# Optimization experiments

Hardware: AMD Instinct MI355X
Metric: run time of the kernel (lower is better)

## Reference

```python
import jax, jax.numpy as jnp
import numpy as np

N, C, H, W = 4, 128, 128, 128
G, K, PAD, DIL = 4, 3, 1, 1
P = K * K
HID = 4 * C
EPS = 1e-6


def ln(x, w, b):
    m = jnp.mean(x, -1, keepdims=True)
    v = jnp.mean((x - m) ** 2, -1, keepdims=True)
    return (x - m) * jax.lax.rsqrt(v + EPS) * w + b


def linear(x, w, b):
    return x @ w.T + b


def grid_sample_zeros(img, grid):
    # img: (B,Hi,Wi,Cc); grid: (B,L,P,2) xy in [-1,1]; bilinear, zeros padding, align_corners=False
    B, Hi, Wi, Cc = img.shape
    gx = (grid[..., 0] + 1.0) * (Wi * 0.5) - 0.5
    gy = (grid[..., 1] + 1.0) * (Hi * 0.5) - 0.5
    x0 = jnp.floor(gx)
    y0 = jnp.floor(gy)
    wx1 = gx - x0
    wy1 = gy - y0
    flat = img.reshape(B, Hi * Wi, Cc)
    Bq, L, Pq = gx.shape

    def tap(yy, xx, wgt):
        valid = (xx >= 0) & (xx <= Wi - 1) & (yy >= 0) & (yy <= Hi - 1)
        idx = (jnp.clip(yy, 0, Hi - 1) * Wi + jnp.clip(xx, 0, Wi - 1)).astype(jnp.int32)
        v = jnp.take_along_axis(flat, idx.reshape(B, L * Pq)[..., None], axis=1)
        return v.reshape(B, L, Pq, Cc) * (wgt * valid)[..., None]

    return (tap(y0, x0, (1 - wx1) * (1 - wy1))
            + tap(y0, x0 + 1, wx1 * (1 - wy1))
            + tap(y0 + 1, x0, (1 - wx1) * wy1)
            + tap(y0 + 1, x0 + 1, wx1 * wy1))


def dcn_core(x, offset, mask):
    # faithful port of dcnv3_core_pytorch (stride=1, offset_scale=1.0)
    n, h, w, c = x.shape
    gc = c // G
    xp = jnp.pad(x, ((0, 0), (PAD, PAD), (PAD, PAD), (0, 0)))
    hi, wi = h + 2 * PAD, w + 2 * PAD
    base = (DIL * (K - 1)) // 2 + 0.5
    ref_y = (base + jnp.arange(h, dtype=jnp.float32)) / hi
    ref_x = (base + jnp.arange(w, dtype=jnp.float32)) / wi
    ref = jnp.stack([jnp.broadcast_to(ref_x[None, :], (h, w)),
                     jnp.broadcast_to(ref_y[:, None], (h, w))], -1)  # (h,w,2) xy
    ks = jnp.arange(K, dtype=jnp.float32) * DIL - (DIL * (K - 1)) // 2
    gxk, gyk = jnp.meshgrid(ks, ks, indexing='ij')  # x slow, y fast (torch meshgrid order)
    grid = jnp.tile(jnp.stack([gxk / wi, gyk / hi], -1).reshape(P, 2), (G, 1))  # (G*P,2)
    sn = jnp.array([wi, hi], jnp.float32)
    loc = ref[None, :, :, None, :] + grid[None, None, None] + offset.reshape(n, h, w, G * P, 2) / sn
    sg = (2.0 * loc - 1.0).reshape(n, h * w, G, P, 2).transpose(0, 2, 1, 3, 4).reshape(n * G, h * w, P, 2)
    img = xp.reshape(n, hi, wi, G, gc).transpose(0, 3, 1, 2, 4).reshape(n * G, hi, wi, gc)
    samp = grid_sample_zeros(img, sg)  # (n*G, h*w, P, gc)
    m = mask.reshape(n, h * w, G, P).transpose(0, 2, 1, 3).reshape(n * G, h * w, P)
    out = jnp.einsum('blpc,blp->blc', samp, m)
    return out.reshape(n, G, h * w, gc).transpose(0, 2, 1, 3).reshape(n, h, w, c)


def dcn_forward(xcl, dw_w, dw_b, dwln_w, dwln_b, off_w, off_b, mask_w, mask_b, outproj_w, outproj_b):
    n, h, w, c = xcl.shape
    y = jax.lax.conv_general_dilated(xcl.transpose(0, 3, 1, 2), dw_w, (1, 1),
                                     ((PAD, PAD), (PAD, PAD)),
                                     dimension_numbers=('NCHW', 'OIHW', 'NCHW'),
                                     feature_group_count=C)
    y = y + dw_b[None, :, None, None]
    x1 = jax.nn.gelu(ln(y.transpose(0, 2, 3, 1), dwln_w, dwln_b), approximate=False)
    offset = linear(x1, off_w, off_b)
    m = jax.nn.softmax(linear(x1, mask_w, mask_b).reshape(n, h, w, G, P), -1).reshape(n, h, w, G * P)
    out = dcn_core(x1, offset, m)
    return linear(out, outproj_w, outproj_b)


def setup_inputs():
    key = jax.random.key(0)
    ks = jax.random.split(key, 8)
    s = 0.02
    return {
        "x": jax.random.normal(ks[0], (N, C, H, W), jnp.float32),
        "norm1_w": jnp.ones((C,), jnp.float32), "norm1_b": jnp.zeros((C,), jnp.float32),
        "dw_w": jax.random.normal(ks[1], (C, 1, K, K), jnp.float32) * 0.1,
        "dw_b": jnp.zeros((C,), jnp.float32),
        "dwln_w": jnp.ones((C,), jnp.float32), "dwln_b": jnp.zeros((C,), jnp.float32),
        "off_w": jax.random.normal(ks[2], (G * P * 2, C), jnp.float32) * 0.05,
        "off_b": jax.random.normal(ks[3], (G * P * 2,), jnp.float32) * 0.5,
        "mask_w": jax.random.normal(ks[4], (G * P, C), jnp.float32) * 0.05,
        "mask_b": jnp.zeros((G * P,), jnp.float32),
        "outproj_w": jax.random.normal(ks[5], (C, C), jnp.float32) * s,
        "outproj_b": jnp.zeros((C,), jnp.float32),
        "norm2_w": jnp.ones((C,), jnp.float32), "norm2_b": jnp.zeros((C,), jnp.float32),
        "fc1_w": jax.random.normal(ks[6], (HID, C), jnp.float32) * s,
        "fc1_b": jnp.zeros((HID,), jnp.float32),
        "fc2_w": jax.random.normal(ks[7], (C, HID), jnp.float32) * s,
        "fc2_b": jnp.zeros((C,), jnp.float32),
    }


def reference(x, norm1_w, norm1_b, dw_w, dw_b, dwln_w, dwln_b, off_w, off_b,
              mask_w, mask_b, outproj_w, outproj_b, norm2_w, norm2_b,
              fc1_w, fc1_b, fc2_w, fc2_b):
    # pre-norm branch (layer_scale=None, post_norm=False, res_post_norm=False, drop_path=Identity)
    xcl = ln(x.transpose(0, 2, 3, 1), norm1_w, norm1_b)  # channels_first -> channels_last LN
    d = dcn_forward(xcl, dw_w, dw_b, dwln_w, dwln_b, off_w, off_b, mask_w, mask_b, outproj_w, outproj_b)
    x = x + d.transpose(0, 3, 1, 2)
    y = ln(x.transpose(0, 2, 3, 1), norm2_w, norm2_b)
    y = linear(jax.nn.gelu(linear(y, fc1_w, fc1_b), approximate=False), fc2_w, fc2_b)
    return x + y.transpose(0, 3, 1, 2)
```

## Files before the change

### kernel.cpp

```cpp
#include <hip/hip_runtime.h>

typedef unsigned short ushort_t;
typedef short short8 __attribute__((ext_vector_type(8)));
typedef float f32x4 __attribute__((ext_vector_type(4)));
typedef ushort_t ushort8v __attribute__((ext_vector_type(8)));
typedef ushort_t ushort4v __attribute__((ext_vector_type(4)));

#define HWsz 16384
#define NHWsz 65536
#define YS 136

__device__ __forceinline__ float b2f(ushort_t u){ return __uint_as_float(((unsigned)u)<<16); }
__device__ __forceinline__ ushort_t f2b(float f){
  unsigned x = __float_as_uint(f);
  x += 0x7fffu + ((x>>16)&1u);
  return (ushort_t)(x>>16);
}
__device__ __forceinline__ float gelu_fast(float x){
  float t = x*x;
  float e = __expf(x*(1.5957691216f + 0.0713548163f*t));
  return x - x*__builtin_amdgcn_rcpf(1.0f + e);
}

#define H16(p, b) ((p)*512 + ((b) ^ (((p)&7)<<4)))
#define XSW(p, b) ((p)*256 + ((b) ^ (((p)&7)<<4)))

__global__ __launch_bounds__(256) void kW_cvt(const float* __restrict__ w1, const float* __restrict__ w2,
    const float* __restrict__ offw, const float* __restrict__ maskw, const float* __restrict__ dww,
    const float* __restrict__ pw, const float* __restrict__ offb, const float* __restrict__ mb,
    ushort_t* __restrict__ w1b, ushort_t* __restrict__ w2b, ushort_t* __restrict__ owmb,
    float* __restrict__ dwwT, ushort_t* __restrict__ pwh, ushort_t* __restrict__ pwl,
    float* __restrict__ obm){
  int i = blockIdx.x*256 + threadIdx.x;
  w1b[i] = f2b(w1[i]);
  w2b[i] = f2b(w2[i]);
  if (i < 16384){
    int row = i >> 7, k = i & 127;
    float v = 0.f;
    if (row < 72) v = offw[row*128 + k];
    else if (row < 108) v = maskw[(row-72)*128 + k];
    owmb[i] = f2b(v);
    float pv = pw[i];
    ushort_t hi = f2b(pv);
    pwh[i] = hi;
    pwl[i] = f2b(pv - b2f(hi));
  }
  if (i < 1152){
    int k = i >> 7, c = i & 127;
    dwwT[i] = dww[c*9 + k];
  }
  if (i < 128){
    obm[i] = (i < 72) ? offb[i] : ((i < 108) ? mb[i-72] : 0.f);
  }
}

__global__ __launch_bounds__(256) void kA_ln1(const float* __restrict__ x,
    const float* __restrict__ w, const float* __restrict__ b,
    ushort_t* __restrict__ xcl){
  __shared__ float tile[128*66];
  __shared__ float psum[256], psq[256];
  __shared__ float ms[64], rs[64];
  int t = threadIdx.x;
  int pos0 = blockIdx.x * 64;
  int n = pos0 >> 14, hw0 = pos0 & 16383;
  const float* xb = x + (size_t)n*128*HWsz + hw0;
  for (int i=0;i<32;i++){
    int e = i*256+t;
    int c = e>>6, p = e&63;
    tile[c*66+p] = xb[(size_t)c*HWsz + p];
  }
  __syncthreads();
  {
    int part = t>>6, p = t&63;
    float s=0.f, q=0.f;
    for (int c=part*32; c<part*32+32; c++){ float v = tile[c*66+p]; s+=v; q+=v*v; }
    psum[part*64+p]=s; psq[part*64+p]=q;
  }
  __syncthreads();
  if (t<64){
    float s=psum[t]+psum[64+t]+psum[128+t]+psum[192+t];
    float q=psq[t]+psq[64+t]+psq[128+t]+psq[192+t];
    float m = s*(1.0f/128.0f);
    float v = q*(1.0f/128.0f)-m*m;
    ms[t]=m; rs[t]=rsqrtf(v+1e-6f);
  }
  __syncthreads();
  for (int i=0;i<32;i++){
    int e = i*256+t;
    int p = e>>7, c = e&127;
    float v = (tile[c*66+p]-ms[p])*rs[p]*w[c]+b[c];
    xcl[(size_t)(pos0+p)*128 + c] = f2b(v);
  }
}

__global__ __launch_bounds__(256) void kB_dw(const ushort_t* __restrict__ xcl,
    const float* __restrict__ dwwT, const float* __restrict__ dwb,
    const float* __restrict__ lnw, const float* __restrict__ lnb,
    ushort_t* __restrict__ x1){
  __shared__ float partS[16*17], partQ[16*17];
  __shared__ float ms[16], rs[16];
  int t = threadIdx.x;
  int pos0 = blockIdx.x*16;
  int n = pos0>>14, hw0 = pos0&16383, h = hw0>>7, w0 = hw0&127;
  int pp = t>>4, l = t&15, ch0 = l*8;
  int w = w0 + pp;
  float acc[8];
  {
    float4 b0 = *(const float4*)(dwb + ch0);
    float4 b1 = *(const float4*)(dwb + ch0 + 4);
    acc[0]=b0.x; acc[1]=b0.y; acc[2]=b0.z; acc[3]=b0.w;
    acc[4]=b1.x; acc[5]=b1.y; acc[6]=b1.z; acc[7]=b1.w;
  }
  #pragma unroll
  for (int kh=0; kh<3; kh++){
    int hy = h + kh - 1;
    if ((unsigned)hy < 128u){
      #pragma unroll
      for (int kw=0; kw<3; kw++){
        int wx = w + kw - 1;
        if ((unsigned)wx < 128u){
          ushort8v xv = *(const ushort8v*)(xcl + ((size_t)(n*16384 + hy*128 + wx))*128 + ch0);
          const float* wr = dwwT + (kh*3+kw)*128 + ch0;
          float4 w0v = *(const float4*)(wr);
          float4 w1v = *(const float4*)(wr+4);
          acc[0] += b2f(xv[0])*w0v.x; acc[1] += b2f(xv[1])*w0v.y;
          acc[2] += b2f(xv[2])*w0v.z; acc[3] += b2f(xv[3])*w0v.w;
          acc[4] += b2f(xv[4])*w1v.x; acc[5] += b2f(xv[5])*w1v.y;
          acc[6] += b2f(xv[6])*w1v.z; acc[7] += b2f(xv[7])*w1v.w;
        }
      }
    }
  }
  {
    float s=0.f, q=0.f;
    #pragma unroll
    for (int j=0;j<8;j++){ s+=acc[j]; q+=acc[j]*acc[j]; }
    partS[pp*17+l]=s; partQ[pp*17+l]=q;
  }
  __syncthreads();
  {
    int p = t>>4, j = t&15;
    float s = partS[p*17+j];
    float q = partQ[p*17+j];
    s += __shfl_xor(s, 1);  q += __shfl_xor(q, 1);
    s += __shfl_xor(s, 2);  q += __shfl_xor(q, 2);
    s += __shfl_xor(s, 4);  q += __shfl_xor(q, 4);
    s += __shfl_xor(s, 8);  q += __shfl_xor(q, 8);
    if (j == 0){
      float m = s*(1.0f/128.0f);
      float var = q*(1.0f/128.0f) - m*m;
      ms[p]=m; rs[p]=rsqrtf(var+1e-6f);
    }
  }
  __syncthreads();
  {
    float m = ms[pp], r = rs[pp];
    float4 lw0 = *(const float4*)(lnw + ch0);
    float4 lw1 = *(const float4*)(lnw + ch0 + 4);
    float4 lb0 = *(const float4*)(lnb + ch0);
    float4 lb1 = *(const float4*)(lnb + ch0 + 4);
    float lw[8] = {lw0.x,lw0.y,lw0.z,lw0.w,lw1.x,lw1.y,lw1.z,lw1.w};
    float lb[8] = {lb0.x,lb0.y,lb0.z,lb0.w,lb1.x,lb1.y,lb1.z,lb1.w};
    ushort8v o;
    #pragma unroll
    for (int j=0;j<8;j++){
      float v = (acc[j]-m)*r*lw[j]+lb[j];
      o[j] = f2b(gelu_fast(v));
    }
    *(ushort8v*)(x1 + (size_t)(pos0+pp)*128 + ch0) = o;
  }
}

#define RS 120
__global__ __launch_bounds__(256) void kCD_dcn(const ushort_t* __restrict__ x1,
    const ushort_t* __restrict__ owmb, const float* __restrict__ obm,
    ushort_t* __restrict__ dcnout){
  __shared__ __align__(16) ushort_t xLb[16*YS];
  __shared__ float raw[16*RS];
  __shared__ __align__(16) float descW[576*4];
  __shared__ __align__(16) int   descO[576*4];
  int t = threadIdx.x;
  int pos0 = blockIdx.x*16;
  int n = pos0>>14, hw0 = pos0&16383, h = hw0>>7, w0 = hw0&127;
  const size_t imgbase = (size_t)n*16384*128;

  *(ushort8v*)(xLb + (t>>4)*YS + (t&15)*8) = *(const ushort8v*)(x1 + (size_t)pos0*128 + t*8);
  __syncthreads();

  {
    int wave = t>>6, lane = t&63;
    int ma = lane&15, quad = lane>>4;
    short8 afrag[4];
    #pragma unroll
    for (int ks=0; ks<4; ks++)
      afrag[ks] = *(const short8*)(xLb + ma*YS + ks*32 + quad*8);
    f32x4 acc[2];
    acc[0] = (f32x4){0.f,0.f,0.f,0.f};
    acc[1] = (f32x4){0.f,0.f,0.f,0.f};
    #pragma unroll
    for (int tile=0; tile<2; tile++){
      const ushort_t* brow = owmb + (size_t)(wave*32 + tile*16 + ma)*128 + quad*8;
      #pragma unroll
      for (int ks=0; ks<4; ks++){
        short8 bfrag = *(const short8*)(brow + ks*32);
        acc[tile] = __builtin_amdgcn_mfma_f32_16x16x32_bf16(bfrag, afrag[ks], acc[tile], 0,0,0);
      }
    }
    #pragma unroll
    for (int tile=0; tile<2; tile++){
      int row0 = wave*32 + tile*16 + quad*4;
      if (row0 < 112){
        f32x4 bias4 = *(const f32x4*)(obm + row0);
        f32x4 o;
        #pragma unroll
        for (int r=0;r<4;r++) o[r] = acc[tile][r] + bias4[r];
        *(f32x4*)(raw + ma*RS + row0) = o;
      }
    }
  }
  __syncthreads();

  if (t < 64){
    int p = t>>2, g = t&3;
    float* mr = raw + p*RS + 72 + g*9;
    float mx = -1e30f;
    for (int q=0;q<9;q++) mx = fmaxf(mx, mr[q]);
    float e[9]; float ssum=0.f;
    for (int q=0;q<9;q++){ e[q]=expf(mr[q]-mx); ssum+=e[q]; }
    float inv = 1.0f/ssum;
    for (int q=0;q<9;q++) mr[q] = e[q]*inv;
  }
  __syncthreads();

  for (int it=0; it<3; it++){
    int tid = t + 256*it;
    if (tid < 576){
      int pp = tid/36, rem = tid - pp*36;
      int g = rem/9, p = rem - g*9;
      int i = p/3, j = p - i*3;
      float ox = raw[pp*RS + 2*(g*9+p)];
      float oy = raw[pp*RS + 2*(g*9+p)+1];
      float mval = raw[pp*RS + 72 + g*9 + p];
      float px = (float)(w0 + pp + i - 1) + ox;
      float py = (float)(h + j - 1) + oy;
      float fx0 = floorf(px), fy0 = floorf(py);
      int ix0 = (int)fx0, iy0 = (int)fy0;
      float fx = px - fx0, fy = py - fy0;
      float vx0 = ((unsigned)ix0     < 128u) ? 1.f : 0.f;
      float vx1 = ((unsigned)(ix0+1) < 128u) ? 1.f : 0.f;
      float vy0 = ((unsigned)iy0     < 128u) ? 1.f : 0.f;
      float vy1 = ((unsigned)(iy0+1) < 128u) ? 1.f : 0.f;
      int cx0 = min(max(ix0,0),127), cx1 = min(max(ix0+1,0),127);
      int cy0 = min(max(iy0,0),127), cy1 = min(max(iy0+1,0),127);
      float4 wv;
      wv.x = (1.f-fx)*(1.f-fy)*mval*vx0*vy0;
      wv.y = fx*(1.f-fy)*mval*vx1*vy0;
      wv.z = (1.f-fx)*fy*mval*vx0*vy1;
      wv.w = fx*fy*mval*vx1*vy1;
      int4 ov;
      ov.x = (cy0*128+cx0)*128;
      ov.y = (cy0*128+cx1)*128;
      ov.z = (cy1*128+cx0)*128;
      ov.w = (cy1*128+cx1)*128;
      *(float4*)(descW + tid*4) = wv;
      *(int4*)(descO + tid*4) = ov;
    }
  }
  __syncthreads();

  {
    int pp = t>>4, l = t&15;
    int ch0 = l*8, g = l>>2;
    const ushort_t* ib = x1 + imgbase + ch0;
    float acc[8];
    #pragma unroll
    for (int j=0;j<8;j++) acc[j]=0.f;
    int dbase = pp*36 + g*9;
    #pragma unroll
    for (int p=0;p<9;p++){
      float4 wv = *(const float4*)(descW + (dbase+p)*4);
      int4  ov = *(const int4*)(descO + (dbase+p)*4);
      ushort8v v00 = *(const ushort8v*)(ib + ov.x);
      ushort8v v10 = *(const ushort8v*)(ib + ov.y);
      ushort8v v01 = *(const ushort8v*)(ib + ov.z);
      ushort8v v11 = *(const ushort8v*)(ib + ov.w);
      #pragma unroll
      for (int j=0;j<8;j++){
        float s = wv.x*b2f(v00[j]) + wv.y*b2f(v10[j]) + wv.z*b2f(v01[j]) + wv.w*b2f(v11[j]);
        acc[j] += s;
      }
    }
    ushort8v outv;
    #pragma unroll
    for (int j=0;j<8;j++) outv[j] = f2b(acc[j]);
    *(ushort8v*)(dcnout + (size_t)(pos0+pp)*128 + ch0) = outv;
  }
}

__global__ __launch_bounds__(256, 6) void kEFG(const ushort_t* __restrict__ dcnout,
    const ushort_t* __restrict__ pwh, const ushort_t* __restrict__ pwl,
    const float* __restrict__ pb, const float* __restrict__ x,
    const float* __restrict__ n2w, const float* __restrict__ n2b,
    const ushort_t* __restrict__ w1b, const float* __restrict__ b1,
    const ushort_t* __restrict__ w2b, const float* __restrict__ b2,
    float* __restrict__ out){
  __shared__ __align__(16) char hidb[16*1024];
  __shared__ __align__(16) char xnb[32*256];
  float* partS = (float*)hidb;
  float* partQ = partS + 32*17;
  float* msh   = partQ + 32*17;
  float* rsh   = msh + 32;

  int t = threadIdx.x;
  int pos0 = blockIdx.x*32;
  int n = pos0>>14, hw0 = pos0&16383;
  int wave = t>>6, lane = t&63;
  int ma = lane&15, quad = lane>>4;

  short8 af[2][4];
  #pragma unroll
  for (int mt=0; mt<2; mt++)
    #pragma unroll
    for (int ks=0; ks<4; ks++)
      af[mt][ks] = *(const short8*)(dcnout + (size_t)(pos0+mt*16+ma)*128 + ks*32 + quad*8);

  f32x4 acc[2][2];
  #pragma unroll
  for (int i=0;i<2;i++){ acc[i][0]=(f32x4){0.f,0.f,0.f,0.f}; acc[i][1]=(f32x4){0.f,0.f,0.f,0.f}; }
  #pragma unroll
  for (int tile=0; tile<2; tile++){
    int c0 = wave*32 + tile*16;
    const ushort_t* bh = pwh + (size_t)(c0 + ma)*128 + quad*8;
    const ushort_t* bl = pwl + (size_t)(c0 + ma)*128 + quad*8;
    #pragma unroll
    for (int ks=0; ks<4; ks++){
      short8 bfh = *(const short8*)(bh + ks*32);
      short8 bfl = *(const short8*)(bl + ks*32);
      #pragma unroll
      for (int mt=0; mt<2; mt++){
        acc[tile][mt] = __builtin_amdgcn_mfma_f32_16x16x32_bf16(bfh, af[mt][ks], acc[tile][mt], 0,0,0);
        acc[tile][mt] = __builtin_amdgcn_mfma_f32_16x16x32_bf16(bfl, af[mt][ks], acc[tile][mt], 0,0,0);
      }
    }
  }

  ushort4v vbp[2][2];
  float sAcc[2], qAcc[2];
  sAcc[0]=0.f; sAcc[1]=0.f; qAcc[0]=0.f; qAcc[1]=0.f;
  #pragma unroll
  for (int tile=0; tile<2; tile++){
    int c0 = wave*32 + tile*16 + quad*4;
    f32x4 bias4 = *(const f32x4*)(pb + c0);
    #pragma unroll
    for (int mt=0; mt<2; mt++){
      int p = mt*16 + ma;
      ushort4v ov;
      #pragma unroll
      for (int r=0;r<4;r++){
        float res = x[((size_t)(n*128) + c0 + r)*HWsz + hw0 + p];
        float v = acc[tile][mt][r] + bias4[r] + res;
        ushort_t ub = f2b(v);
        ov[r] = ub;
        float vv = b2f(ub);
        sAcc[mt] += vv; qAcc[mt] += vv*vv;
      }
      vbp[tile][mt] = ov;
    }
  }
  #pragma unroll
  for (int mt=0; mt<2; mt++){
    int p = mt*16 + ma;
    partS[p*17 + wave*4 + quad] = sAcc[mt];
    partQ[p*17 + wave*4 + quad] = qAcc[mt];
  }
  __syncthreads();
  {
    int p = t>>3, j = t&7;
    float s = partS[p*17 + 2*j] + partS[p*17 + 2*j + 1];
    float q = partQ[p*17 + 2*j] + partQ[p*17 + 2*j + 1];
    s += __shfl_xor(s, 1);  q += __shfl_xor(q, 1);
    s += __shfl_xor(s, 2);  q += __shfl_xor(q, 2);
    s += __shfl_xor(s, 4);  q += __shfl_xor(q, 4);
    if (j == 0){
      float m = s*(1.0f/128.0f);
      float var = q*(1.0f/128.0f) - m*m;
      msh[p] = m; rsh[p] = rsqrtf(var+1e-6f);
    }
  }
  __syncthreads();

  #pragma unroll
  for (int tile=0; tile<2; tile++){
    int c0 = wave*32 + tile*16 + quad*4;
    f32x4 w4 = *(const f32x4*)(n2w + c0);
    f32x4 b4 = *(const f32x4*)(n2b + c0);
    #pragma unroll
    for (int mt=0; mt<2; mt++){
      int p = mt*16 + ma;
      float m = msh[p], r = rsh[p];
      ushort4v nv;
      #pragma unroll
      for (int rr=0;rr<4;rr++) nv[rr] = f2b((b2f(vbp[tile][mt][rr])-m)*r*w4[rr] + b4[rr]);
      *(ushort4v*)(xnb + XSW(p, c0*2)) = nv;
    }
  }
  __syncthreads();

  short8 axf[2][4];
  #pragma unroll
  for (int ks=0; ks<4; ks++)
    #pragma unroll
    for (int mt=0; mt<2; mt++)
      axf[mt][ks] = *(const short8*)(xnb + XSW(mt*16+ma, ks*64 + quad*16));

  f32x4 acc2[2][2];
  acc2[0][0]=(f32x4){0.f,0.f,0.f,0.f}; acc2[0][1]=(f32x4){0.f,0.f,0.f,0.f};
  acc2[1][0]=(f32x4){0.f,0.f,0.f,0.f}; acc2[1][1]=(f32x4){0.f,0.f,0.f,0.f};

  #pragma unroll
  for (int half=0; half<2; half++){
    #pragma unroll
    for (int tt=0; tt<4; tt++){
      int n0g = half*256 + wave*64 + tt*16;
      const ushort_t* brow = w1b + (size_t)(n0g + ma)*128 + quad*8;
      short8 bf[4];
      #pragma unroll
      for (int ks=0; ks<4; ks++) bf[ks] = *(const short8*)(brow + ks*32);
      f32x4 a0 = (f32x4){0.f,0.f,0.f,0.f};
      f32x4 a1 = (f32x4){0.f,0.f,0.f,0.f};
      #pragma unroll
      for (int ks=0; ks<4; ks++){
        a0 = __builtin_amdgcn_mfma_f32_16x16x32_bf16(bf[ks], axf[0][ks], a0, 0,0,0);
        a1 = __builtin_amdgcn_mfma_f32_16x16x32_bf16(bf[ks], axf[1][ks], a1, 0,0,0);
      }
      f32x4 bias4 = *(const f32x4*)(b1 + n0g + quad*4);
      ushort4v hv0, hv1;
      #pragma unroll
      for (int r=0;r<4;r++){
        hv0[r] = f2b(gelu_fast(a0[r] + bias4[r]));
        hv1[r] = f2b(gelu_fast(a1[r] + bias4[r]));
      }
      int nloc = wave*64 + tt*16 + quad*4;
      *(ushort4v*)(hidb + H16(ma,    nloc*2)) = hv0;
      *(ushort4v*)(hidb + H16(16+ma, nloc*2)) = hv1;
    }
    __syncthreads();

    const ushort_t* wb0 = w2b + (size_t)(wave*32 + ma)*512 + half*256 + quad*8;
    const ushort_t* wb1 = wb0 + 16*512;
    #pragma unroll
    for (int ksl=0; ksl<8; ksl++){
      short8 wc0 = *(const short8*)(wb0 + ksl*32);
      short8 wc1 = *(const short8*)(wb1 + ksl*32);
      short8 hc0 = *(const short8*)(hidb + H16(ma,    ksl*64 + quad*16));
      short8 hc1 = *(const short8*)(hidb + H16(16+ma, ksl*64 + quad*16));
      acc2[0][0] = __builtin_amdgcn_mfma_f32_16x16x32_bf16(wc0, hc0, acc2[0][0], 0,0,0);
      acc2[0][1] = __builtin_amdgcn_mfma_f32_16x16x32_bf16(wc0, hc1, acc2[0][1], 0,0,0);
      acc2[1][0] = __builtin_amdgcn_mfma_f32_16x16x32_bf16(wc1, hc0, acc2[1][0], 0,0,0);
      acc2[1][1] = __builtin_amdgcn_mfma_f32_16x16x32_bf16(wc1, hc1, acc2[1][1], 0,0,0);
    }
    if (half == 0) __syncthreads();
  }

  #pragma unroll
  for (int tile=0; tile<2; tile++){
    int c0 = wave*32 + tile*16 + quad*4;
    f32x4 bias4 = *(const f32x4*)(b2 + c0);
    #pragma unroll
    for (int mt=0; mt<2; mt++){
      int p = mt*16 + ma;
      #pragma unroll
      for (int r=0;r<4;r++){
        float v = acc2[tile][mt][r] + bias4[r] + b2f(vbp[tile][mt][r]);
        out[((size_t)(n*128) + c0 + r)*HWsz + hw0 + p] = v;
      }
    }
  }
}

extern "C" void kernel_launch(void* const* d_in, const int* in_sizes, int n_in,
                              void* d_out, int out_size, void* d_ws, size_t ws_size,
                              hipStream_t stream){
  const float* x     = (const float*)d_in[0];
  const float* n1w   = (const float*)d_in[1];
  const float* n1b   = (const float*)d_in[2];
  const float* dww   = (const float*)d_in[3];
  const float* dwb   = (const float*)d_in[4];
  const float* dwlnw = (const float*)d_in[5];
  const float* dwlnb = (const float*)d_in[6];
  const float* offw  = (const float*)d_in[7];
  const float* offb  = (const float*)d_in[8];
  const float* maskw = (const float*)d_in[9];
  const float* maskb = (const float*)d_in[10];
  const float* pw    = (const float*)d_in[11];
  const float* pb    = (const float*)d_in[12];
  const float* n2w   = (const float*)d_in[13];
  const float* n2b   = (const float*)d_in[14];
  const float* w1    = (const float*)d_in[15];
  const float* b1    = (const float*)d_in[16];
  const float* w2    = (const float*)d_in[17];
  const float* b2    = (const float*)d_in[18];

  char* wsb = (char*)d_ws;
  ushort_t* R0   = (ushort_t*)(wsb);
  ushort_t* R1   = (ushort_t*)(wsb + (16u<<20));
  ushort_t* w1b  = (ushort_t*)(wsb + (32u<<20));
  ushort_t* w2b  = (ushort_t*)(wsb + (32u<<20) + (128u<<10));
  ushort_t* owmb = (ushort_t*)(wsb + (32u<<20) + (256u<<10));
  ushort_t* pwh  = (ushort_t*)(wsb + (32u<<20) + (288u<<10));
  ushort_t* pwl  = (ushort_t*)(wsb + (32u<<20) + (320u<<10));
  float*    dwwT = (float*)(wsb + (32u<<20) + (352u<<10));
  float*    obm  = (float*)(wsb + (32u<<20) + (358u<<10));
  float* out = (float*)d_out;

  hipLaunchKernelGGL(kW_cvt,  dim3(256),   dim3(256), 0, stream, w1, w2, offw, maskw, dww, pw, offb, maskb, w1b, w2b, owmb, dwwT, pwh, pwl, obm);
  hipLaunchKernelGGL(kA_ln1,  dim3(1024),  dim3(256), 0, stream, x, n1w, n1b, R0);
  hipLaunchKernelGGL(kB_dw,   dim3(4096),  dim3(256), 0, stream, R0, dwwT, dwb, dwlnw, dwlnb, R1);
  hipLaunchKernelGGL(kCD_dcn, dim3(4096),  dim3(256), 0, stream, R1, owmb, obm, R0);
  hipLaunchKernelGGL(kEFG,    dim3(2048),  dim3(256), 0, stream, R0, pwh, pwl, pb, x, n2w, n2b, w1b, b1, w2b, b2, out);
}
```

Measured before the change: 299.1 us.

## Restructure MLP into two 16-row passes over full hidden width

The fused MLP kernel now handles its 32 positions as two 16-position passes. Each pass computes all 512 hidden units at once into a 16x1024-byte swizzled LDS buffer, then runs the full fc2 reduction over K=512. Before, it split the hidden dimension into two halves for all 32 positions. The change halves live accumulator registers and drops the minimum-occupancy hint from 6 to 4. In exchange, the fc1 and fc2 weight fragments are reloaded from global/L2 for each pass, which halves weight reuse per load.

```diff
diff --git a/kernel.cpp b/kernel.cpp
--- a/kernel.cpp
+++ b/kernel.cpp
@@ -22,8 +22,8 @@
   return x - x*__builtin_amdgcn_rcpf(1.0f + e);
 }
 
-#define H16(p, b) ((p)*512 + ((b) ^ (((p)&7)<<4)))
-#define XSW(p, b) ((p)*256 + ((b) ^ (((p)&7)<<4)))
+#define HSW(p, b) ((p)*1024 + ((b) ^ (((p)&7)<<4)))
+#define XSW(p, b) ((p)*256  + ((b) ^ (((p)&7)<<4)))
 
 __global__ __launch_bounds__(256) void kW_cvt(const float* __restrict__ w1, const float* __restrict__ w2,
     const float* __restrict__ offw, const float* __restrict__ maskw, const float* __restrict__ dww,
@@ -297,7 +297,7 @@
   }
 }
 
-__global__ __launch_bounds__(256, 6) void kEFG(const ushort_t* __restrict__ dcnout,
+__global__ __launch_bounds__(256, 4) void kEFG(const ushort_t* __restrict__ dcnout,
     const ushort_t* __restrict__ pwh, const ushort_t* __restrict__ pwl,
     const float* __restrict__ pb, const float* __restrict__ x,
     const float* __restrict__ n2w, const float* __restrict__ n2b,
@@ -406,75 +406,57 @@
   }
   __syncthreads();
 
-  short8 axf[2][4];
-  #pragma unroll
-  for (int ks=0; ks<4; ks++)
-    #pragma unroll
-    for (int mt=0; mt<2; mt++)
-      axf[mt][ks] = *(const short8*)(xnb + XSW(mt*16+ma, ks*64 + quad*16));
-
-  f32x4 acc2[2][2];
-  acc2[0][0]=(f32x4){0.f,0.f,0.f,0.f}; acc2[0][1]=(f32x4){0.f,0.f,0.f,0.f};
-  acc2[1][0]=(f32x4){0.f,0.f,0.f,0.f}; acc2[1][1]=(f32x4){0.f,0.f,0.f,0.f};
-
-  #pragma unroll
-  for (int half=0; half<2; half++){
-    #pragma unroll
-    for (int tt=0; tt<4; tt++){
-      int n0g = half*256 + wave*64 + tt*16;
+  #pragma unroll
+  for (int ph=0; ph<2; ph++){
+    short8 axf[4];
+    #pragma unroll
+    for (int ks=0; ks<4; ks++)
+      axf[ks] = *(const short8*)(xnb + XSW(ph*16+ma, ks*64 + quad*16));
+    #pragma unroll
+    for (int tt=0; tt<8; tt++){
+      int n0g = wave*128 + tt*16;
       const ushort_t* brow = w1b + (size_t)(n0g + ma)*128 + quad*8;
       short8 bf[4];
       #pragma unroll
       for (int ks=0; ks<4; ks++) bf[ks] = *(const short8*)(brow + ks*32);
       f32x4 a0 = (f32x4){0.f,0.f,0.f,0.f};
-      f32x4 a1 = (f32x4){0.f,0.f,0.f,0.f};
-      #pragma unroll
-      for (int ks=0; ks<4; ks++){
-        a0 = __builtin_amdgcn_mfma_f32_16x16x32_bf16(bf[ks], axf[0][ks], a0, 0,0,0);
-        a1 = __builtin_amdgcn_mfma_f32_16x16x32_bf16(bf[ks], axf[1][ks], a1, 0,0,0);
-      }
-      f32x4 bias4 = *(const f32x4*)(b1 + n0g + quad*4);
-      ushort4v hv0, hv1;
-      #pragma unroll
-      for (int r=0;r<4;r++){
-        hv0[r] = f2b(gelu_fast(a0[r] + bias4[r]));
-        hv1[r] = f2b(gelu_fast(a1[r] + bias4[r]));
-      }
-      int nloc = wave*64 + tt*16 + quad*4;
-      *(ushort4v*)(hidb + H16(ma,    nloc*2)) = hv0;
-      *(ushort4v*)(hidb + H16(16+ma, nloc*2)) = hv1;
+      #pragma unroll
+      for (int ks=0; ks<4; ks++)
+        a0 = __builtin_amdgcn_mfma_f32_16x16x32_bf16(bf[ks], axf[ks], a0, 0,0,0);
+      int n0 = n0g + quad*4;
+      f32x4 bias4 = *(const f32x4*)(b1 + n0);
+      ushort4v hv;
+      #pragma unroll
+      for (int r=0;r<4;r++) hv[r] = f2b(gelu_fast(a0[r] + bias4[r]));
+      *(ushort4v*)(hidb + HSW(ma, n0*2)) = hv;
     }
     __syncthreads();
 
-    const ushort_t* wb0 = w2b + (size_t)(wave*32 + ma)*512 + half*256 + quad*8;
+    f32x4 acc2[2];
+    acc2[0]=(f32x4){0.f,0.f,0.f,0.f}; acc2[1]=(f32x4){0.f,0.f,0.f,0.f};
+    const ushort_t* wb0 = w2b + (size_t)(wave*32 + ma)*512 + quad*8;
     const ushort_t* wb1 = wb0 + 16*512;
     #pragma unroll
-    for (int ksl=0; ksl<8; ksl++){
+    for (int ksl=0; ksl<16; ksl++){
       short8 wc0 = *(const short8*)(wb0 + ksl*32);
       short8 wc1 = *(const short8*)(wb1 + ksl*32);
-      short8 hc0 = *(const short8*)(hidb + H16(ma,    ksl*64 + quad*16));
-      short8 hc1 = *(const short8*)(hidb + H16(16+ma, ksl*64 + quad*16));
-      acc2[0][0] = __builtin_amdgcn_mfma_f32_16x16x32_bf16(wc0, hc0, acc2[0][0], 0,0,0);
-      acc2[0][1] = __builtin_amdgcn_mfma_f32_16x16x32_bf16(wc0, hc1, acc2[0][1], 0,0,0);
-      acc2[1][0] = __builtin_amdgcn_mfma_f32_16x16x32_bf16(wc1, hc0, acc2[1][0], 0,0,0);
-      acc2[1][1] = __builtin_amdgcn_mfma_f32_16x16x32_bf16(wc1, hc1, acc2[1][1], 0,0,0);
-    }
-    if (half == 0) __syncthreads();
-  }
-
-  #pragma unroll
-  for (int tile=0; tile<2; tile++){
-    int c0 = wave*32 + tile*16 + quad*4;
-    f32x4 bias4 = *(const f32x4*)(b2 + c0);
-    #pragma unroll
-    for (int mt=0; mt<2; mt++){
-      int p = mt*16 + ma;
+      short8 hc  = *(const short8*)(hidb + HSW(ma, ksl*64 + quad*16));
+      acc2[0] = __builtin_amdgcn_mfma_f32_16x16x32_bf16(wc0, hc, acc2[0], 0,0,0);
+      acc2[1] = __builtin_amdgcn_mfma_f32_16x16x32_bf16(wc1, hc, acc2[1], 0,0,0);
+    }
+
+    #pragma unroll
+    for (int tile=0; tile<2; tile++){
+      int c0 = wave*32 + tile*16 + quad*4;
+      f32x4 bias4 = *(const f32x4*)(b2 + c0);
+      int p = ph*16 + ma;
       #pragma unroll
       for (int r=0;r<4;r++){
-        float v = acc2[tile][mt][r] + bias4[r] + b2f(vbp[tile][mt][r]);
+        float v = acc2[tile][r] + bias4[r] + b2f(vbp[tile][ph][r]);
         out[((size_t)(n*128) + c0 + r)*HWsz + hw0 + p] = v;
       }
     }
+    if (ph == 0) __syncthreads();
   }
 }
 
```

Result: slower. 334.0 us (+11.7%).
